# Kernel tuning notes

Measured on AMD Instinct MI355X. Metric: run time of the kernel, lower is better.

The kernel has to match this reference:

```python
import jax, jax.numpy as jnp
import numpy as np

NEG_SLOPE = 0.2  # PyG GATConv default


def gat_layer(x, src, dst, W, a_src, a_dst, bias, n_nodes, heads, out_c, concat):
    # x: [N, F_in]; W: [F_in, heads*out_c]; a_src/a_dst: [heads, out_c]
    h = (x @ W).reshape(n_nodes, heads, out_c)            # [N,H,C]
    alpha_src = jnp.einsum('nhc,hc->nh', h, a_src)         # [N,H]
    alpha_dst = jnp.einsum('nhc,hc->nh', h, a_dst)         # [N,H]
    logits = jax.nn.leaky_relu(alpha_src[src] + alpha_dst[dst], NEG_SLOPE)  # [E,H]
    # segment softmax over incoming edges of each dst node
    m = jax.ops.segment_max(logits, dst, num_segments=n_nodes)
    ex = jnp.exp(logits - m[dst])
    denom = jax.ops.segment_sum(ex, dst, num_segments=n_nodes)
    alpha = ex / denom[dst]                                # [E,H]
    msg = h[src] * alpha[:, :, None]                       # [E,H,C]
    out = jax.ops.segment_sum(msg, dst, num_segments=n_nodes)  # [N,H,C]
    if concat:
        out = out.reshape(n_nodes, heads * out_c)
    else:
        out = out.mean(axis=1)
    return out + bias


def setup_inputs() -> dict:
    key = jax.random.key(0)
    ks = jax.random.split(key, 12)
    N, E, F_IN, OUT_C, NG = 50000, 1600000, 64, 32, 512
    H1, C1 = 4, 32
    x = jax.random.normal(ks[0], (N, F_IN), dtype=jnp.float32)
    edge_index = jax.random.randint(ks[1], (2, E), 0, N, dtype=jnp.int64)
    batch = jnp.sort(jax.random.randint(ks[2], (N,), 0, NG, dtype=jnp.int64))
    s1 = 1.0 / np.sqrt(F_IN)
    W1 = jax.random.uniform(ks[3], (F_IN, H1 * C1), jnp.float32, -s1, s1)
    a_src1 = jax.random.uniform(ks[4], (H1, C1), jnp.float32, -s1, s1)
    a_dst1 = jax.random.uniform(ks[5], (H1, C1), jnp.float32, -s1, s1)
    b1 = jnp.zeros((H1 * C1,), jnp.float32)
    s2 = 1.0 / np.sqrt(H1 * C1)
    W2 = jax.random.uniform(ks[6], (H1 * C1, OUT_C), jnp.float32, -s2, s2)
    a_src2 = jax.random.uniform(ks[7], (1, OUT_C), jnp.float32, -s2, s2)
    a_dst2 = jax.random.uniform(ks[8], (1, OUT_C), jnp.float32, -s2, s2)
    b2 = jnp.zeros((OUT_C,), jnp.float32)
    return {"x": x, "edge_index": edge_index, "batch": batch, "num_graphs": NG,
            "W1": W1, "a_src1": a_src1, "a_dst1": a_dst1, "b1": b1,
            "W2": W2, "a_src2": a_src2, "a_dst2": a_dst2, "b2": b2}


def reference(x, edge_index, batch, num_graphs, W1, a_src1, a_dst1, b1, W2, a_src2, a_dst2, b2):
    N = x.shape[0]
    loops = jnp.arange(N, dtype=edge_index.dtype)
    src = jnp.concatenate([edge_index[0], loops])  # add_self_loops=True (PyG default)
    dst = jnp.concatenate([edge_index[1], loops])
    h = gat_layer(x, src, dst, W1, a_src1, a_dst1, b1, N, 4, 32, True)
    h = jax.nn.elu(h)
    h = gat_layer(h, src, dst, W2, a_src2, a_dst2, b2, N, 1, 32, False)
    # global_mean_pool over graph ids
    sums = jax.ops.segment_sum(h, batch, num_segments=num_graphs)
    counts = jax.ops.segment_sum(jnp.ones((N,), h.dtype), batch, num_segments=num_graphs)
    return sums / jnp.maximum(counts, 1.0)[:, None]
```

## Files before the change

### kernel.cpp

```cpp
#include <hip/hip_runtime.h>
#include <hip/hip_bf16.h>

#define N_NODES     50000
#define N_EDGES     1600000
#define N_TOT_EDGES (N_EDGES + N_NODES)
#define NUM_GRAPHS  512
#define F_IN        64
#define F1          128
#define C2          32
#define NEG_SLOPE   0.2f

#define BSH         6
#define NB          ((N_NODES + 63) >> 6)
#define BIN_T       256
#define EPB         8192
#define NBLK        ((N_TOT_EDGES + EPB - 1) / EPB)
#define EPT         (EPB / BIN_T)
#define CAPB        2560
#define CAP         6144
#define G1B         (N_NODES / 8)

typedef __hip_bfloat16 bf16;
typedef unsigned int uint32;
typedef unsigned short ushort;
typedef float fp2 __attribute__((ext_vector_type(2)));

static __device__ __forceinline__ float bf2f(bf16 v) { return __bfloat162float(v); }
static __device__ __forceinline__ float bflo(uint32 u) { return __uint_as_float(u << 16); }
static __device__ __forceinline__ float bfhi(uint32 u) { return __uint_as_float(u & 0xFFFF0000u); }

#define FP8LO(w) ((fp2)__builtin_amdgcn_cvt_pk_f32_fp8((w), false))
#define FP8HI(w) ((fp2)__builtin_amdgcn_cvt_pk_f32_fp8((w), true))
static __device__ __forceinline__ unsigned char f2fp8(float v) {
    return (unsigned char)(__builtin_amdgcn_cvt_pk_fp8_f32(v, v, 0, false) & 0xFF);
}

static __device__ __forceinline__ float fload(const void* p, int i, bool f32) {
    return f32 ? ((const float*)p)[i] : bf2f(((const bf16*)p)[i]);
}
static __device__ __forceinline__ int iload(const void* p, int i, bool i64) {
    return i64 ? (int)((const long long*)p)[i] : ((const int*)p)[i];
}
static __device__ __forceinline__ float lrelu(float l) { return l > 0.f ? l : NEG_SLOPE * l; }
static __device__ __forceinline__ int clampn(int s) {
    return s < 0 ? 0 : (s >= N_NODES ? N_NODES - 1 : s);
}

static __device__ __forceinline__ void accrow(fp2 acc[4], uint4 u, float we) {
    fp2 w2; w2.x = we; w2.y = we;
    fp2 v;
    v.x = bflo(u.x); v.y = bfhi(u.x); acc[0] += w2 * v;
    v.x = bflo(u.y); v.y = bfhi(u.y); acc[1] += w2 * v;
    v.x = bflo(u.z); v.y = bfhi(u.z); acc[2] += w2 * v;
    v.x = bflo(u.w); v.y = bfhi(u.w); acc[3] += w2 * v;
}

static __device__ __forceinline__ void accrow8(fp2 acc[4], uint2 u, float we) {
    fp2 w2; w2.x = we; w2.y = we;
    acc[0] += w2 * FP8LO(u.x);
    acc[1] += w2 * FP8HI(u.x);
    acc[2] += w2 * FP8LO(u.y);
    acc[3] += w2 * FP8HI(u.y);
}

__global__ void sniff_kernel(const ushort* __restrict__ xb, const int* __restrict__ ei,
                             int* __restrict__ flags, int* __restrict__ cursor) {
    int t = threadIdx.x;
    if (t < 16) flags[t] = 0;
    for (int b = t; b < NB; b += 256) cursor[b] = 0;
    __syncthreads();
    int badf = 0;
    for (int i = t; i < 8192; i += 256) {
        int e = (xb[i] >> 7) & 0xFF;
        if (e >= 0xC0) badf = 1;
    }
    if (badf) atomicOr(&flags[0], 1);
    if (ei[2 * t + 1] != 0) atomicOr(&flags[1], 1);
}

__global__ __launch_bounds__(256) void prep_kernel(
    const void* __restrict__ ei, const void* __restrict__ x, const void* __restrict__ W1,
    const void* __restrict__ awS, const void* __restrict__ awD,
    const int* __restrict__ flags,
    int* __restrict__ cursor, uint32* __restrict__ packed,
    unsigned char* __restrict__ h1, float* __restrict__ as1, float* __restrict__ ad1) {
    __shared__ int lcnt[NB];
    __shared__ int loff[NB];
    __shared__ int runB[NB];
    __shared__ float xs[8][F_IN];
    bool f32 = (flags[0] != 0);
    bool i64 = (flags[1] == 0);
    int tid = threadIdx.x;

    if (blockIdx.x < (unsigned)NBLK) {
        for (int b = tid; b < NB; b += BIN_T) { lcnt[b] = 0; loff[b] = 0; }
        __syncthreads();
        int e0 = blockIdx.x * EPB;
        uint32 pkreg[EPT];
#pragma unroll
        for (int it = 0; it < EPT; ++it) {
            int e = e0 + it * BIN_T + tid;
            if (e < N_TOT_EDGES) {
                int s, d;
                if (e < N_EDGES) { s = clampn(iload(ei, e, i64)); d = clampn(iload(ei, N_EDGES + e, i64)); }
                else             { s = d = e - N_EDGES; }
                pkreg[it] = ((uint32)d << 16) | (uint32)s;
                atomicAdd(&lcnt[d >> BSH], 1);
            } else {
                pkreg[it] = 0xFFFFFFFFu;
            }
        }
        __syncthreads();
        for (int b = tid; b < NB; b += BIN_T)
            runB[b] = lcnt[b] ? atomicAdd(&cursor[b], lcnt[b]) : 0;
        __syncthreads();
#pragma unroll
        for (int it = 0; it < EPT; ++it) {
            uint32 pk = pkreg[it];
            if (pk != 0xFFFFFFFFu) {
                int b = pk >> 22;
                int r = runB[b] + atomicAdd(&loff[b], 1);
                if (r >= CAPB) r = CAPB - 1;
                packed[(size_t)b * CAPB + r] = pk;
            }
        }
    } else {
        int n0 = (blockIdx.x - NBLK) * 8;
        int hi = tid >> 7, f = tid & 127;
        if (f32) {
            for (int i = tid; i < 8 * F_IN; i += 256)
                xs[i >> 6][i & 63] = ((const float*)x)[(size_t)n0 * F_IN + i];
        } else {
            const uint32* xu = (const uint32*)x + (size_t)n0 * 32;
            uint32 u = xu[tid];
            int row = tid >> 5, c2 = (tid & 31) * 2;
            xs[row][c2]     = bflo(u);
            xs[row][c2 + 1] = bfhi(u);
        }
        __syncthreads();
        fp2 a0 = {0.f, 0.f}, a1 = {0.f, 0.f}, a2 = {0.f, 0.f}, a3 = {0.f, 0.f};
        const float* xr0 = xs[hi * 4 + 0];
        const float* xr1 = xs[hi * 4 + 1];
        const float* xr2 = xs[hi * 4 + 2];
        const float* xr3 = xs[hi * 4 + 3];
        if (f32) {
            const float* w = (const float*)W1;
#pragma unroll
            for (int k = 0; k < F_IN; k += 2) {
                fp2 wp; wp.x = w[k * F1 + f]; wp.y = w[(k + 1) * F1 + f];
                fp2 x0 = *(const fp2*)&xr0[k];
                fp2 x1 = *(const fp2*)&xr1[k];
                fp2 x2 = *(const fp2*)&xr2[k];
                fp2 x3 = *(const fp2*)&xr3[k];
                a0 += x0 * wp; a1 += x1 * wp; a2 += x2 * wp; a3 += x3 * wp;
            }
        } else {
            const bf16* w = (const bf16*)W1;
#pragma unroll
            for (int k = 0; k < F_IN; k += 2) {
                fp2 wp; wp.x = bf2f(w[k * F1 + f]); wp.y = bf2f(w[(k + 1) * F1 + f]);
                fp2 x0 = *(const fp2*)&xr0[k];
                fp2 x1 = *(const fp2*)&xr1[k];
                fp2 x2 = *(const fp2*)&xr2[k];
                fp2 x3 = *(const fp2*)&xr3[k];
                a0 += x0 * wp; a1 += x1 * wp; a2 += x2 * wp; a3 += x3 * wp;
            }
        }
        float aws = fload(awS, f, f32), awd = fload(awD, f, f32);
        float accs[4] = {a0.x + a0.y, a1.x + a1.y, a2.x + a2.y, a3.x + a3.y};
        int h = (f >> 5), c = f & 31;
#pragma unroll
        for (int j = 0; j < 4; ++j) {
            int n = n0 + hi * 4 + j;
            h1[(size_t)n * F1 + f] = f2fp8(accs[j]);
            float ps = accs[j] * aws, pd = accs[j] * awd;
#pragma unroll
            for (int off = 16; off > 0; off >>= 1) {
                ps += __shfl_down(ps, off, 32);
                pd += __shfl_down(pd, off, 32);
            }
            if (c == 0) {
                as1[n * 4 + h] = ps;
                ad1[n * 4 + h] = pd;
            }
        }
    }
}

__global__ __launch_bounds__(256) void build_kernel(
    const uint32* __restrict__ packed, const int* __restrict__ counts,
    int* __restrict__ rowptr, int* __restrict__ col) {
    __shared__ int red[256];
    __shared__ int ncnt[64];
    __shared__ int nbase[64];
    __shared__ int ncur[64];
    __shared__ int colL[CAP];
    int b = blockIdx.x, tid = threadIdx.x;
    int prt = 0;
    for (int i = tid; i < b; i += 256) prt += counts[i];
    red[tid] = prt;
    __syncthreads();
    for (int off = 128; off > 0; off >>= 1) {
        if (tid < off) red[tid] += red[tid + off];
        __syncthreads();
    }
    int base = red[0];
    int cnt = counts[b];
    if (cnt > CAPB) cnt = CAPB;
    int n0 = b << BSH;
    const uint32* pk = packed + (size_t)b * CAPB;
    if (tid < 64) ncnt[tid] = 0;
    __syncthreads();
    uint32 pkr[(CAPB + 255) / 256];
    int m = 0;
    for (int i = tid; i < cnt; i += 256) {
        pkr[m] = pk[i];
        atomicAdd(&ncnt[(pkr[m] >> 16) & 63], 1);
        ++m;
    }
    __syncthreads();
    if (tid == 0) {
        int run = 0;
        for (int j = 0; j < 64; ++j) { nbase[j] = run; ncur[j] = run; run += ncnt[j]; }
    }
    __syncthreads();
    if (tid < 64 && n0 + tid < N_NODES) rowptr[n0 + tid] = base + nbase[tid];
    if (b == 0 && tid == 96) rowptr[N_NODES] = N_TOT_EDGES;
    bool staged = (cnt <= CAP);
    m = 0;
    for (int i = tid; i < cnt; i += 256) {
        uint32 u = pkr[m++];
        int r = atomicAdd(&ncur[(u >> 16) & 63], 1);
        if (staged) colL[r] = (int)(u & 0xFFFFu);
        else        col[base + r] = (int)(u & 0xFFFFu);
    }
    __syncthreads();
    if (staged)
        for (int i = tid; i < cnt; i += 256) col[base + i] = colL[i];
}

__global__ __launch_bounds__(256) void agg1_kernel(
    const unsigned char* __restrict__ h1, const float* __restrict__ as1, const float* __restrict__ ad1,
    const int* __restrict__ rowptr, const int* __restrict__ col,
    const void* __restrict__ b1, const void* __restrict__ W2,
    const void* __restrict__ aS2w, const void* __restrict__ aD2w,
    const int* __restrict__ flags,
    bf16* __restrict__ h2, float* __restrict__ as2, float* __restrict__ ad2) {
    __shared__ float4 wbuf[4][64];
    __shared__ int    soff[4][64];
    __shared__ float  yL[4][F1];
    __shared__ float  part[4][256];
    bool f32 = (flags[0] != 0);
    int tid = threadIdx.x, lane = tid & 63, wv = tid >> 6;
    int n0 = blockIdx.x * 4;
    int n = n0 + wv;
    int r0 = rowptr[n], r1 = rowptr[n + 1];
    float4 ad = ((const float4*)ad1)[n];
    const char* h1b = (const char*)h1;
    int slot = lane >> 4, cl = lane & 15;
    int hsel = cl >> 2;
    int cl8 = cl * 8;
    const float* wfb = (const float*)&wbuf[wv][0];
    fp2 acc2[4] = {{0.f,0.f},{0.f,0.f},{0.f,0.f},{0.f,0.f}};
    float den = 0.f;

    for (int base = r0; base < r1; base += 64) {
        int cnt = r1 - base; if (cnt > 64) cnt = 64;
        int idx = lane < cnt ? lane : cnt - 1;
        int s = clampn(col[base + idx]);
        float4 a = ((const float4*)as1)[s];
        float4 w;
        w.x = __expf(lrelu(a.x + ad.x));
        w.y = __expf(lrelu(a.y + ad.y));
        w.z = __expf(lrelu(a.z + ad.z));
        w.w = __expf(lrelu(a.w + ad.w));
        wbuf[wv][lane] = w;
        soff[wv][lane] = s << 7;
        __builtin_amdgcn_wave_barrier();
        int i = slot;
        for (; i + 12 < cnt; i += 16) {
            float we0 = wfb[(i     ) * 4 + hsel]; int o0 = soff[wv][i];
            float we1 = wfb[(i +  4) * 4 + hsel]; int o1 = soff[wv][i + 4];
            float we2 = wfb[(i +  8) * 4 + hsel]; int o2 = soff[wv][i + 8];
            float we3 = wfb[(i + 12) * 4 + hsel]; int o3 = soff[wv][i + 12];
            uint2 u0 = *(const uint2*)(h1b + (o0 + cl8));
            uint2 u1 = *(const uint2*)(h1b + (o1 + cl8));
            uint2 u2 = *(const uint2*)(h1b + (o2 + cl8));
            uint2 u3 = *(const uint2*)(h1b + (o3 + cl8));
            accrow8(acc2, u0, we0);
            accrow8(acc2, u1, we1);
            accrow8(acc2, u2, we2);
            accrow8(acc2, u3, we3);
            den += (we0 + we1) + (we2 + we3);
        }
        for (; i < cnt; i += 4) {
            float we = wfb[i * 4 + hsel];
            int o = soff[wv][i];
            uint2 u = *(const uint2*)(h1b + (o + cl8));
            accrow8(acc2, u, we);
            den += we;
        }
        __builtin_amdgcn_wave_barrier();
    }
    float accf[8] = {acc2[0].x, acc2[0].y, acc2[1].x, acc2[1].y,
                     acc2[2].x, acc2[2].y, acc2[3].x, acc2[3].y};
#pragma unroll
    for (int off = 16; off <= 32; off <<= 1) {
#pragma unroll
        for (int j = 0; j < 8; ++j) accf[j] += __shfl_xor(accf[j], off, 64);
        den += __shfl_xor(den, off, 64);
    }
    if (lane < 16) {
        float rd = 1.f / den;
        int c0 = lane * 8;
#pragma unroll
        for (int j = 0; j < 8; ++j) {
            float o = accf[j] * rd + fload(b1, c0 + j, f32);
            yL[wv][c0 + j] = o > 0.f ? o : (__expf(o) - 1.f);
        }
    }
    __syncthreads();
    {
        int c = tid & 31, q = tid >> 5;
        float wr[16];
        if (f32) {
            const float* w = (const float*)W2;
#pragma unroll
            for (int k = 0; k < 16; ++k) wr[k] = w[(q * 16 + k) * C2 + c];
        } else {
            const bf16* w = (const bf16*)W2;
#pragma unroll
            for (int k = 0; k < 16; ++k) wr[k] = bf2f(w[(q * 16 + k) * C2 + c]);
        }
        float p0 = 0.f, p1 = 0.f, p2 = 0.f, p3 = 0.f;
#pragma unroll
        for (int k = 0; k < 16; ++k) {
            int f = q * 16 + k;
            float wvv = wr[k];
            p0 += yL[0][f] * wvv;
            p1 += yL[1][f] * wvv;
            p2 += yL[2][f] * wvv;
            p3 += yL[3][f] * wvv;
        }
        part[0][tid] = p0; part[1][tid] = p1; part[2][tid] = p2; part[3][tid] = p3;
    }
    __syncthreads();
    if (tid < 128) {
        int j = tid >> 5, cc = tid & 31;
        float s = 0.f;
#pragma unroll
        for (int qq = 0; qq < 8; ++qq) s += part[j][qq * 32 + cc];
        h2[(size_t)(n0 + j) * C2 + cc] = __float2bfloat16(s);
        float ps = s * fload(aS2w, cc, f32);
        float pd = s * fload(aD2w, cc, f32);
#pragma unroll
        for (int off = 16; off > 0; off >>= 1) {
            ps += __shfl_down(ps, off, 32);
            pd += __shfl_down(pd, off, 32);
        }
        if (cc == 0) { as2[n0 + j] = ps; ad2[n0 + j] = pd; }
    }
}

__global__ __launch_bounds__(256) void agg2_kernel(
    const bf16* __restrict__ h2, const float* __restrict__ as2, const float* __restrict__ ad2,
    const int* __restrict__ rowptr, const int* __restrict__ col,
    const void* __restrict__ b2, const int* __restrict__ flags, float* __restrict__ v2) {
    __shared__ float wl[4][64];
    __shared__ int   sf[4][64];
    bool f32 = (flags[0] != 0);
    int tid = threadIdx.x, lane = tid & 63, wv = tid >> 6;
    int n = blockIdx.x * 4 + wv;
    int r0 = rowptr[n], r1 = rowptr[n + 1];
    float adn = ad2[n];
    const char* h2b = (const char*)h2;
    int slot = lane >> 2, cl = lane & 3;
    int cl16 = cl * 16;
    fp2 acc2[4] = {{0.f,0.f},{0.f,0.f},{0.f,0.f},{0.f,0.f}};
    float den = 0.f;

    for (int base = r0; base < r1; base += 64) {
        int cnt = r1 - base; if (cnt > 64) cnt = 64;
        int idx = lane < cnt ? lane : cnt - 1;
        int s = clampn(col[base + idx]);
        wl[wv][lane] = __expf(lrelu(as2[s] + adn));
        sf[wv][lane] = s << 6;
        __builtin_amdgcn_wave_barrier();
        int i = slot;
        for (; i + 16 < cnt; i += 32) {
            float w0 = wl[wv][i];        int p0 = sf[wv][i];
            float w1 = wl[wv][i + 16];   int p1 = sf[wv][i + 16];
            uint4 u0 = *(const uint4*)(h2b + (p0 + cl16));
            uint4 u1 = *(const uint4*)(h2b + (p1 + cl16));
            accrow(acc2, u0, w0);
            accrow(acc2, u1, w1);
            den += w0 + w1;
        }
        for (; i < cnt; i += 16) {
            float w = wl[wv][i];
            int p = sf[wv][i];
            uint4 u = *(const uint4*)(h2b + (p + cl16));
            accrow(acc2, u, w);
            den += w;
        }
        __builtin_amdgcn_wave_barrier();
    }
    float accf[8] = {acc2[0].x, acc2[0].y, acc2[1].x, acc2[1].y,
                     acc2[2].x, acc2[2].y, acc2[3].x, acc2[3].y};
#pragma unroll
    for (int off = 4; off <= 32; off <<= 1) {
#pragma unroll
        for (int j = 0; j < 8; ++j) accf[j] += __shfl_xor(accf[j], off, 64);
        den += __shfl_xor(den, off, 64);
    }
    if (lane < 4) {
        float rd = 1.f / den;
        int c0 = lane * 8;
        float4 o0, o1;
        o0.x = accf[0] * rd + fload(b2, c0 + 0, f32);
        o0.y = accf[1] * rd + fload(b2, c0 + 1, f32);
        o0.z = accf[2] * rd + fload(b2, c0 + 2, f32);
        o0.w = accf[3] * rd + fload(b2, c0 + 3, f32);
        o1.x = accf[4] * rd + fload(b2, c0 + 4, f32);
        o1.y = accf[5] * rd + fload(b2, c0 + 5, f32);
        o1.z = accf[6] * rd + fload(b2, c0 + 6, f32);
        o1.w = accf[7] * rd + fload(b2, c0 + 7, f32);
        ((float4*)v2)[(size_t)n * 8 + lane * 2]     = o0;
        ((float4*)v2)[(size_t)n * 8 + lane * 2 + 1] = o1;
    }
}

__global__ __launch_bounds__(64) void pool_kernel(
    const float* __restrict__ v2, const void* __restrict__ batch,
    const int* __restrict__ flags, void* __restrict__ out) {
    bool f32 = (flags[0] != 0);
    bool i64 = (flags[1] == 0);
    int g = blockIdx.x, lane = threadIdx.x;
    int lo = 0, hi = N_NODES;
    while (lo < hi) { int mid = (lo + hi) >> 1; if (iload(batch, mid, i64) < g) lo = mid + 1; else hi = mid; }
    int lo2 = lo, hi2 = N_NODES;
    while (lo2 < hi2) { int mid = (lo2 + hi2) >> 1; if (iload(batch, mid, i64) < g + 1) lo2 = mid + 1; else hi2 = mid; }
    int c = lane & 31, slot = lane >> 5;
    float sum = 0.f;
    for (int nn = lo + slot; nn < lo2; nn += 2) sum += v2[nn * C2 + c];
    sum += __shfl_down(sum, 32, 64);
    if (lane < 32) {
        int cntn = lo2 - lo; if (cntn < 1) cntn = 1;
        float v = sum / (float)cntn;
        if (f32) ((float*)out)[g * C2 + c] = v;
        else     ((bf16*)out)[g * C2 + c] = __float2bfloat16(v);
    }
}

extern "C" void kernel_launch(void* const* d_in, const int* in_sizes, int n_in,
                              void* d_out, int out_size, void* d_ws, size_t ws_size,
                              hipStream_t stream) {
    const void* x   = d_in[0];
    const void* ei  = d_in[1];
    const void* bat = d_in[2];
    const void* W1  = d_in[4];
    const void* aS1 = d_in[5];
    const void* aD1 = d_in[6];
    const void* b1  = d_in[7];
    const void* W2  = d_in[8];
    const void* aS2 = d_in[9];
    const void* aD2 = d_in[10];
    const void* b2  = d_in[11];

    char* p = (char*)d_ws;
    auto alloc = [&](size_t bytes) -> char* {
        char* r = p;
        p += (bytes + 255) & ~size_t(255);
        return r;
    };
    char* regionA = alloc((size_t)N_NODES * F1 * 2);
    char* regionB = alloc((size_t)N_NODES * F1 * 2);
    uint32* packed = (uint32*)alloc((size_t)NB * CAPB * 4);
    unsigned char* h1 = (unsigned char*)regionA;
    bf16*  h2   = (bf16*)regionB;
    float* v2   = (float*)(regionB + (size_t)N_NODES * C2 * 2);
    float* as1    = (float*)alloc((size_t)N_NODES * 4 * 4);
    float* ad1    = (float*)alloc((size_t)N_NODES * 4 * 4);
    float* as2    = (float*)alloc((size_t)N_NODES * 4);
    float* ad2    = (float*)alloc((size_t)N_NODES * 4);
    int*   rowptr = (int*)alloc((size_t)(N_NODES + 1) * 4);
    int*   col    = (int*)alloc((size_t)N_TOT_EDGES * 4);
    int*   cursor = (int*)alloc((size_t)NB * 4);
    int*   flags  = (int*)alloc(64);

    sniff_kernel<<<1, 256, 0, stream>>>((const ushort*)x, (const int*)ei, flags, cursor);

    prep_kernel<<<NBLK + G1B, 256, 0, stream>>>(ei, x, W1, aS1, aD1, flags,
                                                cursor, packed, h1, as1, ad1);
    build_kernel<<<NB, 256, 0, stream>>>(packed, cursor, rowptr, col);

    agg1_kernel<<<N_NODES / 4, 256, 0, stream>>>(h1, as1, ad1, rowptr, col, b1, W2, aS2, aD2,
                                                 flags, h2, as2, ad2);
    agg2_kernel<<<N_NODES / 4, 256, 0, stream>>>(h2, as2, ad2, rowptr, col, b2, flags, v2);
    pool_kernel<<<NUM_GRAPHS, 64, 0, stream>>>(v2, bat, flags, d_out);
}
```

Measured before the change: 245.2 us.

## Precompute per-edge attention weights in CSR build and widen agg1 gathers

Moves the per-edge exp(leaky_relu(as1+ad1)) computation out of agg1 into build_kernel, storing a float4 weight per edge in a new wexp buffer in CSR order. agg1 then reads col and wexp directly, without the LDS staging and wave barriers, and has 8 lanes per row each gathering 16 fp8 bytes instead of 16 lanes each gathering 8. The aim is to cut agg1's redundant as1 gathers and give it wider memory accesses. In exchange it writes and rereads about 26 MB of edge weights, which adds memory traffic, and build_kernel now does random reads of as1 and ad1.

```diff
diff --git a/kernel.cpp b/kernel.cpp
--- a/kernel.cpp
+++ b/kernel.cpp
@@ -55,12 +55,12 @@
     v.x = bflo(u.w); v.y = bfhi(u.w); acc[3] += w2 * v;
 }
 
-static __device__ __forceinline__ void accrow8(fp2 acc[4], uint2 u, float we) {
+static __device__ __forceinline__ void accrow16(fp2 acc[8], uint4 u, float we) {
     fp2 w2; w2.x = we; w2.y = we;
-    acc[0] += w2 * FP8LO(u.x);
-    acc[1] += w2 * FP8HI(u.x);
-    acc[2] += w2 * FP8LO(u.y);
-    acc[3] += w2 * FP8HI(u.y);
+    acc[0] += w2 * FP8LO(u.x); acc[1] += w2 * FP8HI(u.x);
+    acc[2] += w2 * FP8LO(u.y); acc[3] += w2 * FP8HI(u.y);
+    acc[4] += w2 * FP8LO(u.z); acc[5] += w2 * FP8HI(u.z);
+    acc[6] += w2 * FP8LO(u.w); acc[7] += w2 * FP8HI(u.w);
 }
 
 __global__ void sniff_kernel(const ushort* __restrict__ xb, const int* __restrict__ ei,
@@ -189,7 +189,8 @@
 
 __global__ __launch_bounds__(256) void build_kernel(
     const uint32* __restrict__ packed, const int* __restrict__ counts,
-    int* __restrict__ rowptr, int* __restrict__ col) {
+    const float* __restrict__ as1, const float* __restrict__ ad1,
+    int* __restrict__ rowptr, int* __restrict__ col, float* __restrict__ wexp) {
     __shared__ int red[256];
     __shared__ int ncnt[64];
     __shared__ int nbase[64];
@@ -231,8 +232,18 @@
     for (int i = tid; i < cnt; i += 256) {
         uint32 u = pkr[m++];
         int r = atomicAdd(&ncur[(u >> 16) & 63], 1);
-        if (staged) colL[r] = (int)(u & 0xFFFFu);
-        else        col[base + r] = (int)(u & 0xFFFFu);
+        int s = (int)(u & 0xFFFFu);
+        int d = (int)(u >> 16);
+        if (staged) colL[r] = s;
+        else        col[base + r] = s;
+        float4 a = ((const float4*)as1)[s];
+        float4 bd = ((const float4*)ad1)[d];
+        float4 w;
+        w.x = __expf(lrelu(a.x + bd.x));
+        w.y = __expf(lrelu(a.y + bd.y));
+        w.z = __expf(lrelu(a.z + bd.z));
+        w.w = __expf(lrelu(a.w + bd.w));
+        ((float4*)wexp)[base + r] = w;
     }
     __syncthreads();
     if (staged)
@@ -240,14 +251,12 @@
 }
 
 __global__ __launch_bounds__(256) void agg1_kernel(
-    const unsigned char* __restrict__ h1, const float* __restrict__ as1, const float* __restrict__ ad1,
+    const unsigned char* __restrict__ h1, const float* __restrict__ wexp,
     const int* __restrict__ rowptr, const int* __restrict__ col,
     const void* __restrict__ b1, const void* __restrict__ W2,
     const void* __restrict__ aS2w, const void* __restrict__ aD2w,
     const int* __restrict__ flags,
     bf16* __restrict__ h2, float* __restrict__ as2, float* __restrict__ ad2) {
-    __shared__ float4 wbuf[4][64];
-    __shared__ int    soff[4][64];
     __shared__ float  yL[4][F1];
     __shared__ float  part[4][256];
     bool f32 = (flags[0] != 0);
@@ -255,68 +264,55 @@
     int n0 = blockIdx.x * 4;
     int n = n0 + wv;
     int r0 = rowptr[n], r1 = rowptr[n + 1];
-    float4 ad = ((const float4*)ad1)[n];
     const char* h1b = (const char*)h1;
-    int slot = lane >> 4, cl = lane & 15;
-    int hsel = cl >> 2;
-    int cl8 = cl * 8;
-    const float* wfb = (const float*)&wbuf[wv][0];
-    fp2 acc2[4] = {{0.f,0.f},{0.f,0.f},{0.f,0.f},{0.f,0.f}};
+    int slot = lane >> 3, cl = lane & 7;
+    int hsel = cl >> 1;
+    int cl16 = cl * 16;
+    fp2 acc2[8] = {{0.f,0.f},{0.f,0.f},{0.f,0.f},{0.f,0.f},
+                   {0.f,0.f},{0.f,0.f},{0.f,0.f},{0.f,0.f}};
     float den = 0.f;
 
     for (int base = r0; base < r1; base += 64) {
-        int cnt = r1 - base; if (cnt > 64) cnt = 64;
-        int idx = lane < cnt ? lane : cnt - 1;
-        int s = clampn(col[base + idx]);
-        float4 a = ((const float4*)as1)[s];
-        float4 w;
-        w.x = __expf(lrelu(a.x + ad.x));
-        w.y = __expf(lrelu(a.y + ad.y));
-        w.z = __expf(lrelu(a.z + ad.z));
-        w.w = __expf(lrelu(a.w + ad.w));
-        wbuf[wv][lane] = w;
-        soff[wv][lane] = s << 7;
-        __builtin_amdgcn_wave_barrier();
-        int i = slot;
-        for (; i + 12 < cnt; i += 16) {
-            float we0 = wfb[(i     ) * 4 + hsel]; int o0 = soff[wv][i];
-            float we1 = wfb[(i +  4) * 4 + hsel]; int o1 = soff[wv][i + 4];
-            float we2 = wfb[(i +  8) * 4 + hsel]; int o2 = soff[wv][i + 8];
-            float we3 = wfb[(i + 12) * 4 + hsel]; int o3 = soff[wv][i + 12];
-            uint2 u0 = *(const uint2*)(h1b + (o0 + cl8));
-            uint2 u1 = *(const uint2*)(h1b + (o1 + cl8));
-            uint2 u2 = *(const uint2*)(h1b + (o2 + cl8));
-            uint2 u3 = *(const uint2*)(h1b + (o3 + cl8));
-            accrow8(acc2, u0, we0);
-            accrow8(acc2, u1, we1);
-            accrow8(acc2, u2, we2);
-            accrow8(acc2, u3, we3);
-            den += (we0 + we1) + (we2 + we3);
-        }
-        for (; i < cnt; i += 4) {
-            float we = wfb[i * 4 + hsel];
-            int o = soff[wv][i];
-            uint2 u = *(const uint2*)(h1b + (o + cl8));
-            accrow8(acc2, u, we);
-            den += we;
-        }
-        __builtin_amdgcn_wave_barrier();
-    }
-    float accf[8] = {acc2[0].x, acc2[0].y, acc2[1].x, acc2[1].y,
-                     acc2[2].x, acc2[2].y, acc2[3].x, acc2[3].y};
-#pragma unroll
-    for (int off = 16; off <= 32; off <<= 1) {
-#pragma unroll
-        for (int j = 0; j < 8; ++j) accf[j] += __shfl_xor(accf[j], off, 64);
+        int of[8]; float wk[8];
+#pragma unroll
+        for (int k = 0; k < 8; ++k) {
+            int i = base + slot + k * 8;
+            int idx = i < r1 ? i : r1 - 1;
+            of[k] = col[idx] << 7;
+            float wv_ = wexp[idx * 4 + hsel];
+            wk[k] = (i < r1) ? wv_ : 0.f;
+        }
+#pragma unroll
+        for (int k = 0; k < 4; ++k) {
+            uint4 u = *(const uint4*)(h1b + (of[k] + cl16));
+            accrow16(acc2, u, wk[k]);
+            den += wk[k];
+        }
+#pragma unroll
+        for (int k = 4; k < 8; ++k) {
+            uint4 u = *(const uint4*)(h1b + (of[k] + cl16));
+            accrow16(acc2, u, wk[k]);
+            den += wk[k];
+        }
+    }
+#pragma unroll
+    for (int off = 8; off <= 32; off <<= 1) {
+#pragma unroll
+        for (int p = 0; p < 8; ++p) {
+            acc2[p].x += __shfl_xor(acc2[p].x, off, 64);
+            acc2[p].y += __shfl_xor(acc2[p].y, off, 64);
+        }
         den += __shfl_xor(den, off, 64);
     }
-    if (lane < 16) {
+    if (lane < 8) {
         float rd = 1.f / den;
-        int c0 = lane * 8;
-#pragma unroll
-        for (int j = 0; j < 8; ++j) {
-            float o = accf[j] * rd + fload(b1, c0 + j, f32);
-            yL[wv][c0 + j] = o > 0.f ? o : (__expf(o) - 1.f);
+        int c0 = lane * 16;
+#pragma unroll
+        for (int p = 0; p < 8; ++p) {
+            float o0 = acc2[p].x * rd + fload(b1, c0 + 2 * p, f32);
+            float o1 = acc2[p].y * rd + fload(b1, c0 + 2 * p + 1, f32);
+            yL[wv][c0 + 2 * p]     = o0 > 0.f ? o0 : (__expf(o0) - 1.f);
+            yL[wv][c0 + 2 * p + 1] = o1 > 0.f ? o1 : (__expf(o1) - 1.f);
         }
     }
     __syncthreads();
@@ -476,6 +472,7 @@
     char* regionA = alloc((size_t)N_NODES * F1 * 2);
     char* regionB = alloc((size_t)N_NODES * F1 * 2);
     uint32* packed = (uint32*)alloc((size_t)NB * CAPB * 4);
+    float* wexp = (float*)alloc((size_t)N_TOT_EDGES * 4 * 4);
     unsigned char* h1 = (unsigned char*)regionA;
     bf16*  h2   = (bf16*)regionB;
     float* v2   = (float*)(regionB + (size_t)N_NODES * C2 * 2);
@@ -492,9 +489,9 @@
 
     prep_kernel<<<NBLK + G1B, 256, 0, stream>>>(ei, x, W1, aS1, aD1, flags,
                                                 cursor, packed, h1, as1, ad1);
-    build_kernel<<<NB, 256, 0, stream>>>(packed, cursor, rowptr, col);
-
-    agg1_kernel<<<N_NODES / 4, 256, 0, stream>>>(h1, as1, ad1, rowptr, col, b1, W2, aS2, aD2,
+    build_kernel<<<NB, 256, 0, stream>>>(packed, cursor, as1, ad1, rowptr, col, wexp);
+
+    agg1_kernel<<<N_NODES / 4, 256, 0, stream>>>(h1, wexp, rowptr, col, b1, W2, aS2, aD2,
                                                  flags, h2, as2, ad2);
     agg2_kernel<<<N_NODES / 4, 256, 0, stream>>>(h2, as2, ad2, rowptr, col, b2, flags, v2);
     pool_kernel<<<NUM_GRAPHS, 64, 0, stream>>>(v2, bat, flags, d_out);
```

Measured after the change: 282.0 us. +15.0%, slower.
